# Kernel optimization log

Measured on AMD Instinct MI355X. Metric: run time of the kernel, lower is better.

The kernel has to match this reference:

```python
import jax, jax.numpy as jnp
import numpy as np

# Hyperparameters (from init_kwargs)
D_MODEL = 1024
D_STATE = 64
HEADDIM = 64
MIMO_RANK = 2
CHUNK = 128
EXPAND = 2
D_INNER = EXPAND * D_MODEL            # 2048
NHEADS = D_INNER // HEADDIM           # 32
G = MIMO_RANK * D_STATE               # effective state channels per head = 128
D_CONV = 4
D_XBC = D_INNER + 2 * NHEADS * G      # conv channels
D_IN_PROJ = 2 * D_INNER + 2 * NHEADS * G + NHEADS  # [z, x, B, C, dt]


def rmsnorm(x, w, eps=1e-5):
    return x * w * jax.lax.rsqrt(jnp.mean(x * x, axis=-1, keepdims=True) + eps)


def setup_inputs() -> dict:
    key = jax.random.key(0)
    ks = jax.random.split(key, 8)
    B, L = 2, 2048
    x = jax.random.normal(ks[0], (B, L, D_MODEL), jnp.float32)
    norm_w = jnp.ones((D_MODEL,), jnp.float32)
    in_proj_w = jax.random.normal(ks[1], (D_IN_PROJ, D_MODEL), jnp.float32) * 0.02
    conv_w = jax.random.normal(ks[2], (D_XBC, D_CONV), jnp.float32) * 0.2
    conv_b = jnp.zeros((D_XBC,), jnp.float32)
    dt_bias = jax.random.uniform(ks[3], (NHEADS,), jnp.float32, minval=-4.0, maxval=-1.0)
    A_log = jnp.log(jax.random.uniform(ks[4], (NHEADS,), jnp.float32, minval=1.0, maxval=8.0))
    D_skip = jnp.ones((NHEADS,), jnp.float32)
    gnorm_w = jnp.ones((D_INNER,), jnp.float32)
    out_proj_w = jax.random.normal(ks[5], (D_MODEL, D_INNER), jnp.float32) * 0.02
    return dict(x=x, norm_w=norm_w, in_proj_w=in_proj_w, conv_w=conv_w, conv_b=conv_b,
                dt_bias=dt_bias, A_log=A_log, D_skip=D_skip, gnorm_w=gnorm_w,
                out_proj_w=out_proj_w)


def _mamba3(u, in_proj_w, conv_w, conv_b, dt_bias, A_log, D_skip, gnorm_w, out_proj_w):
    B, L, _ = u.shape
    H, P = NHEADS, HEADDIM
    nc = L // CHUNK

    zxbcdt = u @ in_proj_w.T                                   # (B,L,D_IN_PROJ)
    z, xbc, dt_raw = jnp.split(zxbcdt, [D_INNER, D_INNER + D_XBC], axis=-1)

    # causal depthwise conv (width D_CONV) + SiLU on [x, B, C]
    xp = jnp.pad(xbc, ((0, 0), (D_CONV - 1, 0), (0, 0)))
    conv = conv_b + sum(xp[:, k:k + L, :] * conv_w[:, k] for k in range(D_CONV))
    xbc = jax.nn.silu(conv)
    xh, Bm, Cm = jnp.split(xbc, [D_INNER, D_INNER + H * G], axis=-1)

    Xc = xh.reshape(B, nc, CHUNK, H, P)
    Bc = Bm.reshape(B, nc, CHUNK, H, G)
    Cc = Cm.reshape(B, nc, CHUNK, H, G)

    dt = jax.nn.softplus(dt_raw + dt_bias)                     # (B,L,H), positive
    A = -jnp.exp(A_log)                                        # (H,), negative
    dtc = dt.reshape(B, nc, CHUNK, H)
    a = dtc * A                                                # log decay, (B,nc,cs,H)
    cum = jnp.cumsum(a, axis=2)                                # inclusive cumsum within chunk

    # intra-chunk (quadratic, causal) part
    cumT = cum.transpose(0, 1, 3, 2)                           # (B,nc,H,cs)
    diff = cumT[..., :, None] - cumT[..., None, :]             # cum_l - cum_s
    mask = jnp.tril(jnp.ones((CHUNK, CHUNK), bool))
    decay = jnp.where(mask, jnp.exp(jnp.where(mask, diff, 0.0)), 0.0)
    dtT = dtc.transpose(0, 1, 3, 2)                            # (B,nc,H,cs)
    scores = jnp.einsum('bclhg,bcshg->bchls', Cc, Bc) * decay * dtT[:, :, :, None, :]
    Y_intra = jnp.einsum('bchls,bcshp->bclhp', scores, Xc)

    # inter-chunk state recurrence
    w = jnp.exp(cum[:, :, -1:, :] - cum) * dtc                 # (B,nc,cs,H)
    S = jnp.einsum('bcshg,bcshp->bchgp', Bc * w[..., None], Xc)  # chunk states
    dlast = jnp.exp(cum[:, :, -1, :])                          # (B,nc,H) total chunk decay

    def step(carry, inp):
        dl, s = inp
        return dl[:, :, None, None] * carry + s, carry

    init = jnp.zeros((B, H, G, P), u.dtype)
    _, Hprev = jax.lax.scan(step, init, (dlast.transpose(1, 0, 2), S.transpose(1, 0, 2, 3, 4)))
    Hprev = Hprev.transpose(1, 0, 2, 3, 4)                     # (B,nc,H,G,P) state before chunk
    Y_inter = jnp.einsum('bclhg,bchgp->bclhp', Cc * jnp.exp(cum)[..., None], Hprev)

    y = (Y_intra + Y_inter + D_skip[:, None] * Xc).reshape(B, L, D_INNER)
    y = rmsnorm(y * jax.nn.silu(z), gnorm_w)                   # gated RMSNorm
    return y @ out_proj_w.T


def reference(x, norm_w, in_proj_w, conv_w, conv_b, dt_bias, A_log, D_skip, gnorm_w, out_proj_w):
    # pre-norm residual wrapper
    return x + _mamba3(rmsnorm(x, norm_w), in_proj_w, conv_w, conv_b,
                       dt_bias, A_log, D_skip, gnorm_w, out_proj_w)
```

## Files before the change

kernel.cpp:

```cpp
#include <hip/hip_runtime.h>

typedef unsigned short u16;
typedef __attribute__((ext_vector_type(8))) short bf16x8;
typedef __attribute__((ext_vector_type(4))) float f32x4;

#define MFMA16(a,b,c) __builtin_amdgcn_mfma_f32_16x16x32_bf16(a,b,c,0,0,0)

#define DMODEL   1024
#define DINNER   2048
#define NHEADS   32
#define HEADDIM  64
#define GDIM     128
#define DXBC     10240
#define DPROJ    12320
#define CHUNK_L  128
#define NCHUNK   16
#define NROWS    4096

__device__ __forceinline__ float b2f(u16 u){ return __uint_as_float(((unsigned)u)<<16); }
__device__ __forceinline__ u16 f2b(float f){
  unsigned u = __float_as_uint(f);
  u += 0x7fffu + ((u>>16)&1u);
  return (u16)(u>>16);
}

__device__ __forceinline__ void gload_lds16(const void* g, void* l){
  __builtin_amdgcn_global_load_lds(
      (const __attribute__((address_space(1))) unsigned int*)g,
      (__attribute__((address_space(3))) unsigned int*)l, 16, 0, 0);
}

__global__ __launch_bounds__(256) void k_prep(const float* __restrict__ s1, u16* __restrict__ d1, int n1,
                                              const float* __restrict__ s2, u16* __restrict__ d2, int n2,
                                              const float* __restrict__ x, const float* __restrict__ w,
                                              u16* __restrict__ u){
  __shared__ float red[4];
  if (blockIdx.x < 2048){
    int i = blockIdx.x*256 + threadIdx.x;
    int stride = 2048*256;
    int t1 = n1 >> 2, t2 = n2 >> 2;
    for (int j=i; j<t1+t2; j+=stride){
      const float4* sp; uint2* dp; int idx;
      if (j < t1){ sp = (const float4*)s1; dp = (uint2*)d1; idx = j; }
      else       { sp = (const float4*)s2; dp = (uint2*)d2; idx = j - t1; }
      float4 v = sp[idx];
      uint2 o;
      o.x = (unsigned)f2b(v.x) | ((unsigned)f2b(v.y)<<16);
      o.y = (unsigned)f2b(v.z) | ((unsigned)f2b(v.w)<<16);
      dp[idx] = o;
    }
  } else {
    int row = blockIdx.x - 2048, tid = threadIdx.x;
    float4 v = reinterpret_cast<const float4*>(x + (size_t)row*DMODEL)[tid];
    float ss = v.x*v.x + v.y*v.y + v.z*v.z + v.w*v.w;
    #pragma unroll
    for (int off=32; off>0; off>>=1) ss += __shfl_down(ss, off, 64);
    if ((tid&63)==0) red[tid>>6] = ss;
    __syncthreads();
    float tot = red[0]+red[1]+red[2]+red[3];
    float sc = rsqrtf(tot/(float)DMODEL + 1e-5f);
    float4 wv = reinterpret_cast<const float4*>(w)[tid];
    uint2 o;
    o.x = (unsigned)f2b(v.x*wv.x*sc) | ((unsigned)f2b(v.y*wv.y*sc)<<16);
    o.y = (unsigned)f2b(v.z*wv.z*sc) | ((unsigned)f2b(v.w*wv.w*sc)<<16);
    reinterpret_cast<uint2*>(u + (size_t)row*DMODEL)[tid] = o;
  }
}

__global__ __launch_bounds__(512) void k_gemm1_8p(const u16* __restrict__ A,
                                                  const u16* __restrict__ W,
                                                  u16* __restrict__ zb,
                                                  u16* __restrict__ xbc){
  __shared__ __align__(16) u16 lds[65536];
  const int tid  = threadIdx.x;
  const int lane = tid & 63, w = tid >> 6;
  const int wr = w >> 2, wc = w & 3;
  int bid = blockIdx.x;
  int xcd = bid & 7, g = bid >> 3;
  int st  = xcd*6 + (g >> 4);
  int wi  = g & 15;
  int tm  = (st/12)*4 + (wi>>2);
  int tn  = (st%12)*4 + (wi&3);
  const int m0 = tm*256, n0 = tn*256;

  const int srow = w*8 + (lane>>3);
  const int scol = ((lane&7) ^ ((lane>>3)&7))*8;
  const u16* aS = A + (size_t)(m0 + srow)*DMODEL + scol;
  const u16* bS = W + (size_t)(n0 + srow)*DMODEL + scol;
  const int ldsw = w*512;

  const int rr = lane & 15, gq = lane >> 4;

  f32x4 acc[8][4];
  #pragma unroll
  for (int i=0;i<8;i++)
    #pragma unroll
    for (int j=0;j<4;j++) acc[i][j] = (f32x4){0,0,0,0};

  auto SU_A = [&](int kt, int j){
    gload_lds16(aS + (size_t)(j*64)*DMODEL + kt*64,
                lds + (kt&1)*32768 + j*4096 + ldsw);
  };
  auto SU_B = [&](int kt, int j){
    gload_lds16(bS + (size_t)(j*64)*DMODEL + kt*64,
                lds + (kt&1)*32768 + 16384 + j*4096 + ldsw);
  };

  SU_A(0,0); SU_A(0,2); SU_B(0,0); SU_B(0,2); SU_B(0,1); SU_B(0,3); SU_A(0,1); SU_A(0,3);
  asm volatile("s_waitcnt vmcnt(2)" ::: "memory");
  __builtin_amdgcn_s_barrier();
  __builtin_amdgcn_sched_barrier(0);

  for (int kt = 0; kt < 16; ++kt){
    const u16* bufA = lds + (kt&1)*32768;
    const u16* bufB = bufA + 16384;
    const bool stg = (kt < 15);
    bf16x8 af[4][2], bw0[2][2], bw1[2][2];

    auto RDA = [&](int ti, int ks)->bf16x8{
      int r = wr*128 + ti*16 + rr;
      int s = (ks*4 + gq) ^ (rr & 7);
      return *(const bf16x8*)&bufA[r*64 + s*8];
    };
    auto RDB = [&](int tj, int ks)->bf16x8{
      int r = wc*64 + tj*16 + rr;
      int s = (ks*4 + gq) ^ (rr & 7);
      return *(const bf16x8*)&bufB[r*64 + s*8];
    };

    #pragma unroll
    for (int ti=0;ti<4;ti++){ af[ti][0]=RDA(ti,0); af[ti][1]=RDA(ti,1); }
    #pragma unroll
    for (int tj=0;tj<2;tj++){ bw0[tj][0]=RDB(tj,0); bw0[tj][1]=RDB(tj,1); }
    if (stg){ SU_A(kt+1,0); SU_A(kt+1,2); }
    __builtin_amdgcn_s_barrier();
    asm volatile("s_waitcnt lgkmcnt(0)" ::: "memory");
    __builtin_amdgcn_sched_barrier(0);
    __builtin_amdgcn_s_setprio(1);
    #pragma unroll
    for (int ti=0;ti<4;ti++)
      #pragma unroll
      for (int tj=0;tj<2;tj++){
        acc[ti][tj] = MFMA16(af[ti][0], bw0[tj][0], acc[ti][tj]);
        acc[ti][tj] = MFMA16(af[ti][1], bw0[tj][1], acc[ti][tj]);
      }
    __builtin_amdgcn_s_setprio(0);
    __builtin_amdgcn_s_barrier();

    #pragma unroll
    for (int tj=0;tj<2;tj++){ bw1[tj][0]=RDB(tj+2,0); bw1[tj][1]=RDB(tj+2,1); }
    if (stg){ SU_B(kt+1,0); SU_B(kt+1,2); }
    __builtin_amdgcn_s_barrier();
    asm volatile("s_waitcnt lgkmcnt(0)" ::: "memory");
    __builtin_amdgcn_sched_barrier(0);
    __builtin_amdgcn_s_setprio(1);
    #pragma unroll
    for (int ti=0;ti<4;ti++)
      #pragma unroll
      for (int tj=0;tj<2;tj++){
        acc[ti][tj+2] = MFMA16(af[ti][0], bw1[tj][0], acc[ti][tj+2]);
        acc[ti][tj+2] = MFMA16(af[ti][1], bw1[tj][1], acc[ti][tj+2]);
      }
    __builtin_amdgcn_s_setprio(0);
    if (stg) asm volatile("s_waitcnt vmcnt(4)" ::: "memory");
    else     asm volatile("s_waitcnt vmcnt(0)" ::: "memory");
    __builtin_amdgcn_s_barrier();

    #pragma unroll
    for (int ti=0;ti<4;ti++){ af[ti][0]=RDA(ti+4,0); af[ti][1]=RDA(ti+4,1); }
    if (stg){ SU_B(kt+1,1); SU_B(kt+1,3); }
    __builtin_amdgcn_s_barrier();
    asm volatile("s_waitcnt lgkmcnt(0)" ::: "memory");
    __builtin_amdgcn_sched_barrier(0);
    __builtin_amdgcn_s_setprio(1);
    #pragma unroll
    for (int ti=0;ti<4;ti++)
      #pragma unroll
      for (int tj=0;tj<2;tj++){
        acc[4+ti][tj] = MFMA16(af[ti][0], bw0[tj][0], acc[4+ti][tj]);
        acc[4+ti][tj] = MFMA16(af[ti][1], bw0[tj][1], acc[4+ti][tj]);
      }
    __builtin_amdgcn_s_setprio(0);
    __builtin_amdgcn_s_barrier();

    if (stg){ SU_A(kt+1,1); SU_A(kt+1,3); }
    __builtin_amdgcn_s_barrier();
    __builtin_amdgcn_sched_barrier(0);
    __builtin_amdgcn_s_setprio(1);
    #pragma unroll
    for (int ti=0;ti<4;ti++)
      #pragma unroll
      for (int tj=0;tj<2;tj++){
        acc[4+ti][tj+2] = MFMA16(af[ti][0], bw1[tj][0], acc[4+ti][tj+2]);
        acc[4+ti][tj+2] = MFMA16(af[ti][1], bw1[tj][1], acc[4+ti][tj+2]);
      }
    __builtin_amdgcn_s_setprio(0);
    if (stg){
      asm volatile("s_waitcnt vmcnt(2)" ::: "memory");
      __builtin_amdgcn_s_barrier();
      __builtin_amdgcn_sched_barrier(0);
    }
  }

  const int row0 = m0 + wr*128 + (lane>>4)*4;
  const int colb = wc*64 + (lane&15);
  if (tn >= 8){
    const int cb = n0 - DINNER;
    #pragma unroll
    for (int ti=0;ti<8;ti++)
      #pragma unroll
      for (int tj=0;tj<4;tj++)
        #pragma unroll
        for (int q=0;q<4;q++)
          xbc[(size_t)(row0 + ti*16 + q)*DXBC + cb + colb + tj*16] = f2b(acc[ti][tj][q]);
  } else {
    #pragma unroll
    for (int ti=0;ti<8;ti++)
      #pragma unroll
      for (int tj=0;tj<4;tj++)
        #pragma unroll
        for (int q=0;q<4;q++)
          zb[(size_t)(row0 + ti*16 + q)*DINNER + n0 + colb + tj*16] = f2b(acc[ti][tj][q]);
  }
}

__global__ __launch_bounds__(256) void k_gemm_dt(const u16* __restrict__ A,
                                                 const u16* __restrict__ W,
                                                 float* __restrict__ dtraw){
  const int lane = threadIdx.x & 63, wv = threadIdx.x >> 6;
  const int m0 = blockIdx.x*32;
  const int n0 = DINNER + DXBC;
  const int r  = lane & 15;
  const int kb = (lane>>4)*8;
  const int k0 = wv*256;
  const u16* a0p = A + (size_t)(m0 + r)*DMODEL + k0 + kb;
  const u16* a1p = a0p + 16*DMODEL;
  const u16* b0p = W + (size_t)(n0 + r)*DMODEL + k0 + kb;
  const u16* b1p = b0p + 16*DMODEL;
  f32x4 acc00={0,0,0,0}, acc01={0,0,0,0}, acc10={0,0,0,0}, acc11={0,0,0,0};
  #pragma unroll
  for (int k=0;k<256;k+=32){
    bf16x8 a0 = *(const bf16x8*)(a0p + k);
    bf16x8 a1 = *(const bf16x8*)(a1p + k);
    bf16x8 b0 = *(const bf16x8*)(b0p + k);
    bf16x8 b1 = *(const bf16x8*)(b1p + k);
    acc00 = MFMA16(a0,b0,acc00);
    acc01 = MFMA16(a0,b1,acc01);
    acc10 = MFMA16(a1,b0,acc10);
    acc11 = MFMA16(a1,b1,acc11);
  }
  __shared__ float part[4][1024];
  int rowb = (lane>>4)*4, col = lane&15;
  #pragma unroll
  for (int rr=0; rr<4; rr++){
    part[wv][(rowb+rr)*32 + col]         = acc00[rr];
    part[wv][(rowb+rr)*32 + col+16]      = acc01[rr];
    part[wv][(rowb+16+rr)*32 + col]      = acc10[rr];
    part[wv][(rowb+16+rr)*32 + col+16]   = acc11[rr];
  }
  __syncthreads();
  int idx = threadIdx.x*4;
  #pragma unroll
  for (int q=0;q<4;q++){
    int i = idx+q;
    dtraw[(size_t)m0*NHEADS + i] = part[0][i]+part[1][i]+part[2][i]+part[3][i];
  }
}

__global__ __launch_bounds__(256) void k_convdt(const u16* __restrict__ xbc,
                                                const float* __restrict__ cw,
                                                const float* __restrict__ cb,
                                                u16* __restrict__ xh,
                                                u16* __restrict__ Bm,
                                                u16* __restrict__ Cm,
                                                const float* __restrict__ dtraw,
                                                const float* __restrict__ dt_bias,
                                                const float* __restrict__ A_log,
                                                float* __restrict__ dtT,
                                                float* __restrict__ cumT){
  __shared__ float lds2[2][128];
  int tid = threadIdx.x;
  if (blockIdx.x < 2560){
    int cblk = blockIdx.x;
    int cx = cblk % 10, ry = cblk / 10;
    int c0 = (cx*256 + tid)*4;
    int row0 = ry*16;
    int l0 = row0 & 2047;
    float4 w4[4]; float cbv[4];
    #pragma unroll
    for (int j=0;j<4;j++){ w4[j] = reinterpret_cast<const float4*>(cw)[c0+j]; cbv[j] = cb[c0+j]; }
    float p3[4]={0,0,0,0}, p2[4]={0,0,0,0}, p1[4]={0,0,0,0};
    auto loadquad = [&](int rw, float q[4]){
      uint2 v = *(const uint2*)&xbc[(size_t)rw*DXBC + c0];
      const u16* pv = (const u16*)&v;
      #pragma unroll
      for (int j=0;j<4;j++) q[j] = b2f(pv[j]);
    };
    if (l0 >= 3){ loadquad(row0-3,p3); loadquad(row0-2,p2); loadquad(row0-1,p1); }
    #pragma unroll
    for (int i=0;i<16;i++){
      float cur[4]; loadquad(row0+i, cur);
      float o[4];
      #pragma unroll
      for (int j=0;j<4;j++){
        float s = cbv[j] + p3[j]*w4[j].x + p2[j]*w4[j].y + p1[j]*w4[j].z + cur[j]*w4[j].w;
        o[j] = s/(1.f+expf(-s));
      }
      uint2 ov;
      ov.x = (unsigned)f2b(o[0]) | ((unsigned)f2b(o[1])<<16);
      ov.y = (unsigned)f2b(o[2]) | ((unsigned)f2b(o[3])<<16);
      int rw = row0 + i;
      if (c0 < DINNER)            *(uint2*)&xh[(size_t)rw*DINNER + c0] = ov;
      else if (c0 < DINNER+4096)  *(uint2*)&Bm[(size_t)rw*4096 + (c0-DINNER)] = ov;
      else                        *(uint2*)&Cm[(size_t)rw*4096 + (c0-DINNER-4096)] = ov;
      #pragma unroll
      for (int j=0;j<4;j++){ p3[j]=p2[j]; p2[j]=p1[j]; p1[j]=cur[j]; }
    }
  } else {
    int half = tid >> 7;
    int blk  = (blockIdx.x - 2560)*2 + half;
    int h  = blk & 31;
    int bc = blk >> 5;
    int s  = tid & 127;
    int row = bc*128 + s;
    float xv = dtraw[(size_t)row*NHEADS + h] + dt_bias[h];
    float dt = (xv > 20.f) ? xv : log1pf(expf(xv));
    float a  = dt * (-expf(A_log[h]));
    lds2[half][s] = a; __syncthreads();
    #pragma unroll
    for (int off=1; off<128; off<<=1){
      float t = (s>=off) ? lds2[half][s-off] : 0.f;
      __syncthreads();
      lds2[half][s] += t;
      __syncthreads();
    }
    dtT[(size_t)blk*128 + s]  = dt;
    cumT[(size_t)blk*128 + s] = lds2[half][s];
  }
}

__global__ __launch_bounds__(512) void k_states(const u16* __restrict__ Bm,
                                                const u16* __restrict__ xh,
                                                const float* __restrict__ dtT,
                                                const float* __restrict__ cumT,
                                                u16* __restrict__ S){
  int blk = blockIdx.x;
  int h = blk & 31, bc = blk >> 5;
  __shared__ __align__(16) u16 Bw[128][136];
  __shared__ __align__(16) u16 XT[64][136];
  __shared__ float cum[128], dtv[128];
  int tid = threadIdx.x;
  if (tid < 128){ cum[tid] = cumT[(size_t)blk*128+tid]; dtv[tid] = dtT[(size_t)blk*128+tid]; }
  __syncthreads();
  float clast = cum[127];
  #pragma unroll
  for (int it=0; it<4; ++it){
    int s  = it*32 + (tid>>4);
    int g8 = (tid&15)*8;
    uint4 v = *(const uint4*)&Bm[(size_t)(bc*128+s)*4096 + h*128 + g8];
    float w = expf(clast - cum[s]) * dtv[s];
    const u16* pv = (const u16*)&v;
    #pragma unroll
    for (int j=0;j<8;j++) Bw[g8+j][s] = f2b(b2f(pv[j]) * w);
  }
  #pragma unroll
  for (int it=0; it<4; ++it){
    int s  = it*32 + (tid>>4);
    int p4 = (tid&15)*4;
    uint2 v = *(const uint2*)&xh[(size_t)(bc*128+s)*DINNER + h*64 + p4];
    const u16* pv = (const u16*)&v;
    #pragma unroll
    for (int j=0;j<4;j++) XT[p4+j][s] = pv[j];
  }
  __syncthreads();
  int lane = tid & 63, wv = tid >> 6;
  int r = lane & 15, kb = (lane>>4)*8;
  f32x4 acc[4];
  #pragma unroll
  for (int j=0;j<4;j++) acc[j] = (f32x4){0,0,0,0};
  #pragma unroll
  for (int k=0;k<128;k+=32){
    bf16x8 a0 = *(const bf16x8*)&Bw[wv*16 + r][k+kb];
    #pragma unroll
    for (int tj=0;tj<4;tj++){
      bf16x8 bb = *(const bf16x8*)&XT[tj*16 + r][k+kb];
      acc[tj] = MFMA16(a0,bb,acc[tj]);
    }
  }
  u16* Sp = S + (size_t)blk*8192;
  int g0 = wv*16 + (lane>>4)*4, p0 = lane&15;
  #pragma unroll
  for (int tj=0;tj<4;tj++)
    #pragma unroll
    for (int rr=0;rr<4;rr++)
      Sp[(g0 + rr)*64 + tj*16 + p0] = f2b(acc[tj][rr]);
}

__global__ __launch_bounds__(256) void k_scan(const u16* __restrict__ S,
                                              const float* __restrict__ cumT,
                                              u16* __restrict__ Hp){
  int slice = blockIdx.x & 3;
  int bh = blockIdx.x >> 2;
  int b = bh >> 5, h = bh & 31;
  int e0 = slice*2048 + threadIdx.x*8;
  float c8[8];
  #pragma unroll
  for (int j=0;j<8;j++) c8[j] = 0.f;
  int blk0 = (b*16+0)*32 + h;
  uint4 sv = *(const uint4*)&S[(size_t)blk0*8192 + e0];
  float dl = expf(cumT[(size_t)blk0*128 + 127]);
  for (int c=0;c<NCHUNK;c++){
    int blkn = (b*16+c+1)*32 + h;
    uint4 nx; float dln = 0.f;
    if (c < NCHUNK-1){
      nx  = *(const uint4*)&S[(size_t)blkn*8192 + e0];
      dln = expf(cumT[(size_t)blkn*128 + 127]);
    }
    int blk = (b*16+c)*32 + h;
    const u16* sp = (const u16*)&sv;
    uint4 o; u16* op = (u16*)&o;
    #pragma unroll
    for (int j=0;j<8;j++) op[j] = f2b(c8[j]);
    *reinterpret_cast<uint4*>(&Hp[(size_t)blk*8192 + e0]) = o;
    #pragma unroll
    for (int j=0;j<8;j++) c8[j] = dl*c8[j] + b2f(sp[j]);
    sv = nx; dl = dln;
  }
}

__global__ __launch_bounds__(512) void k_intra(const u16* __restrict__ Cm,
                                               const u16* __restrict__ Bm,
                                               const u16* __restrict__ xh,
                                               const u16* __restrict__ Hp,
                                               const float* __restrict__ dtT,
                                               const float* __restrict__ cumT,
                                               const float* __restrict__ Dskip,
                                               u16* __restrict__ yh){
  int blk = blockIdx.x;
  int h = blk & 31, bc = blk >> 5;
  __shared__ __align__(16) u16 Bl[128][136];
  __shared__ __align__(16) u16 XT[64][136];
  __shared__ __align__(16) u16 HT[64][136];
  __shared__ float cum[128], dtv[128];
  int tid = threadIdx.x;
  int lane = tid & 63, wv = tid >> 6;
  int r = lane & 15, kb = (lane>>4)*8;

  bf16x8 cfr[4];
  {
    const u16* cp = Cm + (size_t)(bc*128 + wv*16 + r)*4096 + h*128 + kb;
    #pragma unroll
    for (int ks=0;ks<4;ks++) cfr[ks] = *(const bf16x8*)(cp + ks*32);
  }

  if (tid < 128){ cum[tid] = cumT[(size_t)blk*128+tid]; dtv[tid] = dtT[(size_t)blk*128+tid]; }
  #pragma unroll
  for (int it=0; it<4; ++it){
    int rw = it*32 + (tid>>4);
    int g8 = (tid&15)*8;
    *(uint4*)&Bl[rw][g8] = *(const uint4*)&Bm[(size_t)(bc*128+rw)*4096 + h*128 + g8];
  }
  __syncthreads();

  uint2 xt[4], ht[4];
  #pragma unroll
  for (int it=0; it<4; ++it){
    int s  = it*32 + (tid>>4);
    int p4 = (tid&15)*4;
    xt[it] = *(const uint2*)&xh[(size_t)(bc*128+s)*DINNER + h*64 + p4];
    ht[it] = *(const uint2*)&Hp[(size_t)blk*8192 + (it*32 + (tid>>4))*64 + p4];
  }

  const int tjmax = wv;
  f32x4 p1[8];
  #pragma unroll
  for (int j=0;j<8;j++) p1[j] = (f32x4){0,0,0,0};
  #pragma unroll
  for (int ks=0;ks<4;ks++){
    bf16x8 a0 = cfr[ks];
    #pragma unroll
    for (int tj=0;tj<8;tj++){
      if (tj > tjmax) continue;
      bf16x8 bb = *(const bf16x8*)&Bl[tj*16 + r][ks*32+kb];
      p1[tj] = MFMA16(a0,bb,p1[tj]);
    }
  }
  #pragma unroll
  for (int it=0; it<4; ++it){
    int s  = it*32 + (tid>>4);
    int p4 = (tid&15)*4;
    const u16* pv = (const u16*)&xt[it];
    #pragma unroll
    for (int j=0;j<4;j++) XT[p4+j][s] = pv[j];
    const u16* ph = (const u16*)&ht[it];
    #pragma unroll
    for (int j=0;j<4;j++) HT[p4+j][it*32 + (tid>>4)] = ph[j];
  }
  __syncthreads();

  int row0 = wv*16 + (lane>>4)*4;
  #pragma unroll
  for (int tj=0;tj<8;tj++)
    #pragma unroll
    for (int rr=0;rr<4;rr++){
      int l = row0 + rr;
      int s = tj*16 + (lane&15);
      float v = p1[tj][rr];
      v = (s <= l) ? v * expf(cum[l]-cum[s]) * dtv[s] : 0.f;
      Bl[l][s] = f2b(v);
    }
  __syncthreads();

  f32x4 y[4];
  #pragma unroll
  for (int j=0;j<4;j++) y[j] = (f32x4){0,0,0,0};
  #pragma unroll
  for (int ks=0;ks<4;ks++){
    bf16x8 a0 = cfr[ks];
    #pragma unroll
    for (int tj=0;tj<4;tj++){
      bf16x8 bb = *(const bf16x8*)&HT[tj*16 + r][ks*32+kb];
      y[tj] = MFMA16(a0,bb,y[tj]);
    }
  }
  #pragma unroll
  for (int rr=0;rr<4;rr++){
    float e = expf(cum[row0 + rr]);
    #pragma unroll
    for (int tj=0;tj<4;tj++) y[tj][rr] *= e;
  }
  #pragma unroll
  for (int k=0;k<128;k+=32){
    bf16x8 a0 = *(const bf16x8*)&Bl[wv*16 + r][k+kb];
    #pragma unroll
    for (int tj=0;tj<4;tj++){
      bf16x8 bb = *(const bf16x8*)&XT[tj*16 + r][k+kb];
      y[tj] = MFMA16(a0,bb,y[tj]);
    }
  }
  float Dh = Dskip[h];
  #pragma unroll
  for (int tj=0;tj<4;tj++)
    #pragma unroll
    for (int rr=0;rr<4;rr++){
      int l = row0 + rr;
      int p = tj*16 + (lane&15);
      float xv = b2f(XT[p][l]);
      yh[(size_t)(bc*128 + l)*DINNER + h*64 + p] = f2b(y[tj][rr] + Dh*xv);
    }
}

__global__ __launch_bounds__(256) void k_gate(const u16* __restrict__ yh,
                                              const u16* __restrict__ zb,
                                              const float* __restrict__ gw,
                                              u16* __restrict__ out){
  int row = blockIdx.x, tid = threadIdx.x;
  const uint4 yv = reinterpret_cast<const uint4*>(yh + (size_t)row*DINNER)[tid];
  const uint4 zv = reinterpret_cast<const uint4*>(zb + (size_t)row*DINNER)[tid];
  const unsigned* yp = (const unsigned*)&yv;
  const unsigned* zp = (const unsigned*)&zv;
  float t[8]; float ss = 0.f;
  #pragma unroll
  for (int i=0;i<4;i++){
    float y0 = b2f((u16)yp[i]), y1 = b2f((u16)(yp[i]>>16));
    float z0 = b2f((u16)zp[i]), z1 = b2f((u16)(zp[i]>>16));
    float v0 = y0 * (z0 / (1.f + expf(-z0)));
    float v1 = y1 * (z1 / (1.f + expf(-z1)));
    t[2*i] = v0; t[2*i+1] = v1; ss += v0*v0 + v1*v1;
  }
  #pragma unroll
  for (int off=32; off>0; off>>=1) ss += __shfl_down(ss, off, 64);
  __shared__ float red[4];
  if ((tid&63)==0) red[tid>>6] = ss;
  __syncthreads();
  float tot = red[0]+red[1]+red[2]+red[3];
  float g = rsqrtf(tot/(float)DINNER + 1e-5f);
  const float4 g0 = reinterpret_cast<const float4*>(gw)[tid*2];
  const float4 g1 = reinterpret_cast<const float4*>(gw)[tid*2+1];
  uint4 o;
  unsigned* op = (unsigned*)&o;
  float gg[8] = {g0.x,g0.y,g0.z,g0.w,g1.x,g1.y,g1.z,g1.w};
  #pragma unroll
  for (int i=0;i<4;i++)
    op[i] = (unsigned)f2b(t[2*i]*gg[2*i]*g) | ((unsigned)f2b(t[2*i+1]*gg[2*i+1]*g)<<16);
  reinterpret_cast<uint4*>(out + (size_t)row*DINNER)[tid] = o;
}

__global__ __launch_bounds__(256) void k_gemm2_64(const u16* __restrict__ A,
                                                  const u16* __restrict__ W,
                                                  const float* __restrict__ xres,
                                                  float* __restrict__ out){
  __shared__ __align__(16) u16 lds[2*16384];
  const int tid  = threadIdx.x;
  const int lane = tid & 63, wv = tid >> 6;
  const int wr = wv >> 1, wc = wv & 1;
  const int NWG = 8*32, Q = NWG/8;
  int swz = (blockIdx.x & 7)*Q + (blockIdx.x >> 3);
  int tm = swz / 8, tn = swz % 8;
  int m0 = tm*128, n0 = tn*128;
  const int K = DINNER;

  const int srow = tid >> 3;
  const int sslot = ((tid&7) ^ ((tid>>3)&7))*8;
  const u16* aSrc = A + (size_t)(m0 + srow)*K + sslot;
  const u16* bSrc = W + (size_t)(n0 + srow)*K + sslot;
  const int ldsu = wv*512;

  const int rr = lane & 15, gq = lane >> 4;

  f32x4 acc[4][4];
  #pragma unroll
  for (int i=0;i<4;i++)
    #pragma unroll
    for (int j=0;j<4;j++) acc[i][j] = (f32x4){0,0,0,0};

  auto STAGE = [&](int kt){
    u16* base = lds + (kt&1)*16384;
    #pragma unroll
    for (int j=0;j<4;j++)
      gload_lds16(aSrc + (size_t)(j*32)*K + kt*64, base + j*2048 + ldsu);
    #pragma unroll
    for (int j=0;j<4;j++)
      gload_lds16(bSrc + (size_t)(j*32)*K + kt*64, base + 8192 + j*2048 + ldsu);
  };
  auto KSTEP = [&](int kt, bool stg){
    const u16* bufA = lds + (kt&1)*16384;
    const u16* bufB = bufA + 8192;
    bf16x8 af[4][2], bw[4][2];
    #pragma unroll
    for (int t=0;t<4;t++){
      #pragma unroll
      for (int ks=0;ks<2;ks++){
        int sa = (ks*4 + gq) ^ (rr & 7);
        af[t][ks] = *(const bf16x8*)&bufA[(wr*64 + t*16 + rr)*64 + sa*8];
        bw[t][ks] = *(const bf16x8*)&bufB[(wc*64 + t*16 + rr)*64 + sa*8];
      }
    }
    asm volatile("s_waitcnt lgkmcnt(0)" ::: "memory");
    __builtin_amdgcn_s_barrier();
    if (stg) STAGE(kt+2);
    __builtin_amdgcn_s_setprio(1);
    #pragma unroll
    for (int ti=0;ti<4;ti++)
      #pragma unroll
      for (int tj=0;tj<4;tj++){
        acc[ti][tj] = MFMA16(af[ti][0], bw[tj][0], acc[ti][tj]);
        acc[ti][tj] = MFMA16(af[ti][1], bw[tj][1], acc[ti][tj]);
      }
    __builtin_amdgcn_s_setprio(0);
  };

  STAGE(0); STAGE(1);
  asm volatile("s_waitcnt vmcnt(8)" ::: "memory");
  __builtin_amdgcn_s_barrier();
  __builtin_amdgcn_sched_barrier(0);
  const int NT = K/64;
  for (int kt = 0; kt < NT-2; ++kt){
    KSTEP(kt, true);
    asm volatile("s_waitcnt vmcnt(8)" ::: "memory");
    __builtin_amdgcn_s_barrier();
    __builtin_amdgcn_sched_barrier(0);
  }
  KSTEP(NT-2, false);
  asm volatile("s_waitcnt vmcnt(0)" ::: "memory");
  __builtin_amdgcn_s_barrier();
  __builtin_amdgcn_sched_barrier(0);
  KSTEP(NT-1, false);

  int row0 = m0 + wr*64 + (lane>>4)*4;
  int col0 = n0 + wc*64 + (lane&15);
  #pragma unroll
  for (int ti=0;ti<4;ti++)
    #pragma unroll
    for (int tj=0;tj<4;tj++)
      #pragma unroll
      for (int q=0;q<4;q++){
        size_t idx = (size_t)(row0+ti*16+q)*DMODEL + col0 + tj*16;
        out[idx] = acc[ti][tj][q] + xres[idx];
      }
}

extern "C" void kernel_launch(void* const* d_in, const int* in_sizes, int n_in,
                              void* d_out, int out_size, void* d_ws, size_t ws_size,
                              hipStream_t stream) {
  (void)in_sizes; (void)n_in; (void)out_size; (void)ws_size;
  const float* x         = (const float*)d_in[0];
  const float* norm_w    = (const float*)d_in[1];
  const float* in_proj_w = (const float*)d_in[2];
  const float* conv_w    = (const float*)d_in[3];
  const float* conv_b    = (const float*)d_in[4];
  const float* dt_bias   = (const float*)d_in[5];
  const float* A_log     = (const float*)d_in[6];
  const float* D_skip    = (const float*)d_in[7];
  const float* gnorm_w   = (const float*)d_in[8];
  const float* out_proj_w= (const float*)d_in[9];
  float* out = (float*)d_out;

  char* ws = (char*)d_ws;
  size_t off = 0;
  auto alloc = [&](size_t bytes)->char*{
    char* p = ws + off; off = (off + bytes + 255) & ~(size_t)255; return p;
  };
  u16*   W2    = (u16*)  alloc((size_t)DMODEL*DINNER*2);
  u16*   zb    = (u16*)  alloc((size_t)NROWS*DINNER*2);
  float* dtraw = (float*)alloc((size_t)NROWS*NHEADS*4);
  float* dtT   = (float*)alloc((size_t)1024*128*4);
  float* cumT  = (float*)alloc((size_t)1024*128*4);
  u16*   xhb   = (u16*)  alloc((size_t)NROWS*DINNER*2);
  u16*   Bmb   = (u16*)  alloc((size_t)NROWS*4096*2);
  u16*   Cmb   = (u16*)  alloc((size_t)NROWS*4096*2);
  char*  R1    = alloc((size_t)NROWS*DXBC*2);
  u16*   xbcr  = (u16*)R1;
  u16*   S     = (u16*)R1;
  u16*   Hp    = (u16*)(R1 + (size_t)1024*8192*4);
  u16*   yh    = (u16*)R1;
  char*  R2    = alloc((size_t)DPROJ*DMODEL*2 + (size_t)NROWS*DMODEL*2);
  u16*   W1    = (u16*)R2;
  u16*   u_bf  = (u16*)(R2 + (size_t)DPROJ*DMODEL*2);
  u16*   gated = (u16*)R2;

  k_prep<<<2048+NROWS,256,0,stream>>>(in_proj_w, W1, DPROJ*DMODEL,
                                      out_proj_w, W2, DMODEL*DINNER,
                                      x, norm_w, u_bf);
  k_gemm_dt<<<NROWS/32,256,0,stream>>>(u_bf, W1, dtraw);
  k_gemm1_8p<<<768,512,0,stream>>>(u_bf, W1, zb, xbcr);
  k_convdt<<<2560+512,256,0,stream>>>(xbcr, conv_w, conv_b, xhb, Bmb, Cmb,
                                      dtraw, dt_bias, A_log, dtT, cumT);
  k_states<<<1024,512,0,stream>>>(Bmb, xhb, dtT, cumT, S);
  k_scan<<<256,256,0,stream>>>(S, cumT, Hp);
  k_intra<<<1024,512,0,stream>>>(Cmb, Bmb, xhb, Hp, dtT, cumT, D_skip, yh);
  k_gate<<<NROWS,256,0,stream>>>(yh, zb, gnorm_w, gated);
  k_gemm2_64<<<8*32,256,0,stream>>>(gated, W2, x, out);
}
```

Baseline: 288.0 us.

## Fuse causal conv and SiLU into in_proj GEMM epilogue via LDS tile

The in_proj GEMM epilogue now stages each 256x256 xBC output tile in swizzled LDS and applies the depthwise causal conv plus SiLU directly, writing xh/B/C. This avoids writing and re-reading the full raw xBC activation through global memory. Rows whose conv window crosses a tile boundary (the first three of each tile) are fixed up in a small separate kernel, using boundary rows saved to a side buffer. The fused epilogue does its serial per-column conv loop with strided, uncoalesced global stores and an extra barrier, which may lengthen the GEMM tail.

Result: slower. 417.2 us (+44.8%).

```diff
diff --git a/kernel.cpp b/kernel.cpp
--- a/kernel.cpp
+++ b/kernel.cpp
@@ -70,7 +70,12 @@
 __global__ __launch_bounds__(512) void k_gemm1_8p(const u16* __restrict__ A,
                                                   const u16* __restrict__ W,
                                                   u16* __restrict__ zb,
-                                                  u16* __restrict__ xbc){
+                                                  u16* __restrict__ xh,
+                                                  u16* __restrict__ Bm,
+                                                  u16* __restrict__ Cm,
+                                                  const float* __restrict__ cw,
+                                                  const float* __restrict__ cb,
+                                                  u16* __restrict__ sideRaw){
   __shared__ __align__(16) u16 lds[65536];
   const int tid  = threadIdx.x;
   const int lane = tid & 63, w = tid >> 6;
@@ -202,18 +207,9 @@
     }
   }
 
-  const int row0 = m0 + wr*128 + (lane>>4)*4;
-  const int colb = wc*64 + (lane&15);
-  if (tn >= 8){
-    const int cb = n0 - DINNER;
-    #pragma unroll
-    for (int ti=0;ti<8;ti++)
-      #pragma unroll
-      for (int tj=0;tj<4;tj++)
-        #pragma unroll
-        for (int q=0;q<4;q++)
-          xbc[(size_t)(row0 + ti*16 + q)*DXBC + cb + colb + tj*16] = f2b(acc[ti][tj][q]);
-  } else {
+  if (tn < 8){
+    const int row0 = m0 + wr*128 + (lane>>4)*4;
+    const int colb = wc*64 + (lane&15);
     #pragma unroll
     for (int ti=0;ti<8;ti++)
       #pragma unroll
@@ -221,6 +217,54 @@
         #pragma unroll
         for (int q=0;q<4;q++)
           zb[(size_t)(row0 + ti*16 + q)*DINNER + n0 + colb + tj*16] = f2b(acc[ti][tj][q]);
+    return;
+  }
+
+  const int cb0 = n0 - DINNER;
+  #pragma unroll
+  for (int ti=0;ti<8;ti++)
+    #pragma unroll
+    for (int tj=0;tj<4;tj++)
+      #pragma unroll
+      for (int q=0;q<4;q++){
+        int rl = wr*128 + ti*16 + (lane>>4)*4 + q;
+        int cl = wc*64 + tj*16 + (lane&15);
+        lds[rl*256 + (cl ^ (((rl>>2)&3)<<4))] = f2b(acc[ti][tj][q]);
+      }
+  __syncthreads();
+
+  #pragma unroll
+  for (int it=0; it<3; ++it){
+    int idx = tid + it*512;
+    int r6  = idx >> 8;
+    int c   = idx & 255;
+    int rl  = (r6 < 3) ? r6 : (250 + r6);
+    sideRaw[((size_t)tm*6 + r6)*DXBC + cb0 + c] = lds[rl*256 + (c ^ (((rl>>2)&3)<<4))];
+  }
+
+  {
+    int c    = tid & 255;
+    int half = tid >> 8;
+    int gc   = cb0 + c;
+    float4 w4 = reinterpret_cast<const float4*>(cw)[gc];
+    float cbv = cb[gc];
+    u16* outp; int ostride;
+    if (gc < DINNER){ outp = xh + gc; ostride = DINNER; }
+    else if (gc < DINNER+4096){ outp = Bm + (gc - DINNER); ostride = 4096; }
+    else { outp = Cm + (gc - DINNER - 4096); ostride = 4096; }
+    auto TRD = [&](int l)->float {
+      return b2f(lds[l*256 + (c ^ (((l>>2)&3)<<4))]);
+    };
+    int lstart = half ? 128 : 3;
+    int lend   = half ? 256 : 128;
+    float p3 = TRD(lstart-3), p2 = TRD(lstart-2), p1 = TRD(lstart-1);
+    for (int l=lstart; l<lend; ++l){
+      float cur = TRD(l);
+      float s = cbv + p3*w4.x + p2*w4.y + p1*w4.z + cur*w4.w;
+      s = s/(1.f+expf(-s));
+      outp[(size_t)(m0+l)*ostride] = f2b(s);
+      p3=p2; p2=p1; p1=cur;
+    }
   }
 }
 
@@ -267,58 +311,48 @@
   }
 }
 
-__global__ __launch_bounds__(256) void k_convdt(const u16* __restrict__ xbc,
-                                                const float* __restrict__ cw,
-                                                const float* __restrict__ cb,
-                                                u16* __restrict__ xh,
-                                                u16* __restrict__ Bm,
-                                                u16* __restrict__ Cm,
-                                                const float* __restrict__ dtraw,
-                                                const float* __restrict__ dt_bias,
-                                                const float* __restrict__ A_log,
-                                                float* __restrict__ dtT,
-                                                float* __restrict__ cumT){
+__global__ __launch_bounds__(256) void k_fixdt(const u16* __restrict__ sideRaw,
+                                               const float* __restrict__ cw,
+                                               const float* __restrict__ cb,
+                                               u16* __restrict__ xh,
+                                               u16* __restrict__ Bm,
+                                               u16* __restrict__ Cm,
+                                               const float* __restrict__ dtraw,
+                                               const float* __restrict__ dt_bias,
+                                               const float* __restrict__ A_log,
+                                               float* __restrict__ dtT,
+                                               float* __restrict__ cumT){
   __shared__ float lds2[2][128];
   int tid = threadIdx.x;
-  if (blockIdx.x < 2560){
-    int cblk = blockIdx.x;
-    int cx = cblk % 10, ry = cblk / 10;
-    int c0 = (cx*256 + tid)*4;
-    int row0 = ry*16;
-    int l0 = row0 & 2047;
-    float4 w4[4]; float cbv[4];
-    #pragma unroll
-    for (int j=0;j<4;j++){ w4[j] = reinterpret_cast<const float4*>(cw)[c0+j]; cbv[j] = cb[c0+j]; }
-    float p3[4]={0,0,0,0}, p2[4]={0,0,0,0}, p1[4]={0,0,0,0};
-    auto loadquad = [&](int rw, float q[4]){
-      uint2 v = *(const uint2*)&xbc[(size_t)rw*DXBC + c0];
-      const u16* pv = (const u16*)&v;
-      #pragma unroll
-      for (int j=0;j<4;j++) q[j] = b2f(pv[j]);
-    };
-    if (l0 >= 3){ loadquad(row0-3,p3); loadquad(row0-2,p2); loadquad(row0-1,p1); }
-    #pragma unroll
-    for (int i=0;i<16;i++){
-      float cur[4]; loadquad(row0+i, cur);
-      float o[4];
-      #pragma unroll
-      for (int j=0;j<4;j++){
-        float s = cbv[j] + p3[j]*w4[j].x + p2[j]*w4[j].y + p1[j]*w4[j].z + cur[j]*w4[j].w;
-        o[j] = s/(1.f+expf(-s));
-      }
-      uint2 ov;
-      ov.x = (unsigned)f2b(o[0]) | ((unsigned)f2b(o[1])<<16);
-      ov.y = (unsigned)f2b(o[2]) | ((unsigned)f2b(o[3])<<16);
-      int rw = row0 + i;
-      if (c0 < DINNER)            *(uint2*)&xh[(size_t)rw*DINNER + c0] = ov;
-      else if (c0 < DINNER+4096)  *(uint2*)&Bm[(size_t)rw*4096 + (c0-DINNER)] = ov;
-      else                        *(uint2*)&Cm[(size_t)rw*4096 + (c0-DINNER-4096)] = ov;
-      #pragma unroll
-      for (int j=0;j<4;j++){ p3[j]=p2[j]; p2[j]=p1[j]; p1[j]=cur[j]; }
+  if (blockIdx.x < 16){
+    int tm = blockIdx.x;
+    int m0 = tm*256;
+    bool bstart = (m0 & 2047) == 0;
+    for (int it=0; it<120; ++it){
+      int idx = it*256 + tid;
+      int j  = idx / DXBC;
+      int gc = idx - j*DXBC;
+      float4 w4 = reinterpret_cast<const float4*>(cw)[gc];
+      const float* wk = (const float*)&w4;
+      float s = cb[gc];
+      #pragma unroll
+      for (int k=0;k<4;k++){
+        int i = j - 3 + k;
+        if (bstart && i < 0) continue;
+        u16 rv = (i >= 0) ? sideRaw[((size_t)tm*6 + i)*DXBC + gc]
+                          : sideRaw[((size_t)(tm-1)*6 + (i+6))*DXBC + gc];
+        s += b2f(rv) * wk[k];
+      }
+      s = s/(1.f+expf(-s));
+      u16 ov = f2b(s);
+      int rw = m0 + j;
+      if (gc < DINNER)            xh[(size_t)rw*DINNER + gc] = ov;
+      else if (gc < DINNER+4096)  Bm[(size_t)rw*4096 + (gc-DINNER)] = ov;
+      else                        Cm[(size_t)rw*4096 + (gc-DINNER-4096)] = ov;
     }
   } else {
     int half = tid >> 7;
-    int blk  = (blockIdx.x - 2560)*2 + half;
+    int blk  = (blockIdx.x - 16)*2 + half;
     int h  = blk & 31;
     int bc = blk >> 5;
     int s  = tid & 127;
@@ -709,8 +743,8 @@
   u16*   xhb   = (u16*)  alloc((size_t)NROWS*DINNER*2);
   u16*   Bmb   = (u16*)  alloc((size_t)NROWS*4096*2);
   u16*   Cmb   = (u16*)  alloc((size_t)NROWS*4096*2);
+  u16*   sideRaw=(u16*)  alloc((size_t)16*6*DXBC*2);
   char*  R1    = alloc((size_t)NROWS*DXBC*2);
-  u16*   xbcr  = (u16*)R1;
   u16*   S     = (u16*)R1;
   u16*   Hp    = (u16*)(R1 + (size_t)1024*8192*4);
   u16*   yh    = (u16*)R1;
@@ -723,9 +757,10 @@
                                       out_proj_w, W2, DMODEL*DINNER,
                                       x, norm_w, u_bf);
   k_gemm_dt<<<NROWS/32,256,0,stream>>>(u_bf, W1, dtraw);
-  k_gemm1_8p<<<768,512,0,stream>>>(u_bf, W1, zb, xbcr);
-  k_convdt<<<2560+512,256,0,stream>>>(xbcr, conv_w, conv_b, xhb, Bmb, Cmb,
-                                      dtraw, dt_bias, A_log, dtT, cumT);
+  k_gemm1_8p<<<768,512,0,stream>>>(u_bf, W1, zb, xhb, Bmb, Cmb,
+                                   conv_w, conv_b, sideRaw);
+  k_fixdt<<<16+512,256,0,stream>>>(sideRaw, conv_w, conv_b, xhb, Bmb, Cmb,
+                                   dtraw, dt_bias, A_log, dtT, cumT);
   k_states<<<1024,512,0,stream>>>(Bmb, xhb, dtT, cumT, S);
   k_scan<<<256,256,0,stream>>>(S, cumT, Hp);
   k_intra<<<1024,512,0,stream>>>(Cmb, Bmb, xhb, Hp, dtT, cumT, D_skip, yh);
```

## Stage GEMM epilogues through swizzled LDS and widen conv loads/stores

Applied to the files above, without the earlier changes.

The in-projection GEMM epilogue now writes its bf16 accumulators into LDS with an XOR swizzle, then each thread writes a full row segment with 16-byte vector stores instead of scattered 2-byte stores. The out-projection epilogue does the same in fp32, fusing the residual add with float4 loads and stores. The conv kernel processes 8 channels per thread with 16-byte accesses, halving its block count. This targets uncoalesced narrow global writes, at the cost of an extra LDS round trip, a barrier, and more registers per conv thread.

New measurement: 316.3 us. +9.8%, slower.

```diff
diff --git a/kernel.cpp b/kernel.cpp
--- a/kernel.cpp
+++ b/kernel.cpp
@@ -202,25 +202,30 @@
     }
   }
 
-  const int row0 = m0 + wr*128 + (lane>>4)*4;
-  const int colb = wc*64 + (lane&15);
-  if (tn >= 8){
-    const int cb = n0 - DINNER;
-    #pragma unroll
-    for (int ti=0;ti<8;ti++)
-      #pragma unroll
-      for (int tj=0;tj<4;tj++)
-        #pragma unroll
-        for (int q=0;q<4;q++)
-          xbc[(size_t)(row0 + ti*16 + q)*DXBC + cb + colb + tj*16] = f2b(acc[ti][tj][q]);
-  } else {
-    #pragma unroll
-    for (int ti=0;ti<8;ti++)
-      #pragma unroll
-      for (int tj=0;tj<4;tj++)
-        #pragma unroll
-        for (int q=0;q<4;q++)
-          zb[(size_t)(row0 + ti*16 + q)*DINNER + n0 + colb + tj*16] = f2b(acc[ti][tj][q]);
+  #pragma unroll
+  for (int ti=0;ti<8;ti++)
+    #pragma unroll
+    for (int tj=0;tj<4;tj++)
+      #pragma unroll
+      for (int q=0;q<4;q++){
+        int rl = wr*128 + ti*16 + (lane>>4)*4 + q;
+        int cl = wc*64 + tj*16 + (lane&15);
+        lds[rl*256 + (cl ^ ((rl&7)<<3))] = f2b(acc[ti][tj][q]);
+      }
+  __syncthreads();
+  u16* dst; size_t dstride; int dcol;
+  if (tn >= 8){ dst = xbc; dstride = DXBC;   dcol = n0 - DINNER; }
+  else        { dst = zb;  dstride = DINNER; dcol = n0; }
+  {
+    int r  = tid & 255;
+    int hb = (tid >> 8) * 128;
+    u16* drow = dst + (size_t)(m0 + r)*dstride + dcol + hb;
+    #pragma unroll
+    for (int i=0;i<16;i++){
+      int c = hb + i*8;
+      uint4 v = *(const uint4*)&lds[r*256 + (c ^ ((r&7)<<3))];
+      *(uint4*)&drow[i*8] = v;
+    }
   }
 }
 
@@ -280,45 +285,43 @@
                                                 float* __restrict__ cumT){
   __shared__ float lds2[2][128];
   int tid = threadIdx.x;
-  if (blockIdx.x < 2560){
+  if (blockIdx.x < 1280){
     int cblk = blockIdx.x;
-    int cx = cblk % 10, ry = cblk / 10;
-    int c0 = (cx*256 + tid)*4;
+    int cx = cblk % 5, ry = cblk / 5;
+    int c0 = (cx*256 + tid)*8;
     int row0 = ry*16;
     int l0 = row0 & 2047;
-    float4 w4[4]; float cbv[4];
-    #pragma unroll
-    for (int j=0;j<4;j++){ w4[j] = reinterpret_cast<const float4*>(cw)[c0+j]; cbv[j] = cb[c0+j]; }
-    float p3[4]={0,0,0,0}, p2[4]={0,0,0,0}, p1[4]={0,0,0,0};
-    auto loadquad = [&](int rw, float q[4]){
-      uint2 v = *(const uint2*)&xbc[(size_t)rw*DXBC + c0];
+    float4 w4[8]; float cbv[8];
+    #pragma unroll
+    for (int j=0;j<8;j++){ w4[j] = reinterpret_cast<const float4*>(cw)[c0+j]; cbv[j] = cb[c0+j]; }
+    float p3[8]={0,0,0,0,0,0,0,0}, p2[8]={0,0,0,0,0,0,0,0}, p1[8]={0,0,0,0,0,0,0,0};
+    auto loadoct = [&](int rw, float q[8]){
+      uint4 v = *(const uint4*)&xbc[(size_t)rw*DXBC + c0];
       const u16* pv = (const u16*)&v;
       #pragma unroll
-      for (int j=0;j<4;j++) q[j] = b2f(pv[j]);
+      for (int j=0;j<8;j++) q[j] = b2f(pv[j]);
     };
-    if (l0 >= 3){ loadquad(row0-3,p3); loadquad(row0-2,p2); loadquad(row0-1,p1); }
+    if (l0 >= 3){ loadoct(row0-3,p3); loadoct(row0-2,p2); loadoct(row0-1,p1); }
     #pragma unroll
     for (int i=0;i<16;i++){
-      float cur[4]; loadquad(row0+i, cur);
-      float o[4];
-      #pragma unroll
-      for (int j=0;j<4;j++){
+      float cur[8]; loadoct(row0+i, cur);
+      u16 o[8];
+      #pragma unroll
+      for (int j=0;j<8;j++){
         float s = cbv[j] + p3[j]*w4[j].x + p2[j]*w4[j].y + p1[j]*w4[j].z + cur[j]*w4[j].w;
-        o[j] = s/(1.f+expf(-s));
-      }
-      uint2 ov;
-      ov.x = (unsigned)f2b(o[0]) | ((unsigned)f2b(o[1])<<16);
-      ov.y = (unsigned)f2b(o[2]) | ((unsigned)f2b(o[3])<<16);
+        o[j] = f2b(s/(1.f+expf(-s)));
+      }
+      uint4 ov = *(const uint4*)o;
       int rw = row0 + i;
-      if (c0 < DINNER)            *(uint2*)&xh[(size_t)rw*DINNER + c0] = ov;
-      else if (c0 < DINNER+4096)  *(uint2*)&Bm[(size_t)rw*4096 + (c0-DINNER)] = ov;
-      else                        *(uint2*)&Cm[(size_t)rw*4096 + (c0-DINNER-4096)] = ov;
-      #pragma unroll
-      for (int j=0;j<4;j++){ p3[j]=p2[j]; p2[j]=p1[j]; p1[j]=cur[j]; }
+      if (c0 < DINNER)            *(uint4*)&xh[(size_t)rw*DINNER + c0] = ov;
+      else if (c0 < DINNER+4096)  *(uint4*)&Bm[(size_t)rw*4096 + (c0-DINNER)] = ov;
+      else                        *(uint4*)&Cm[(size_t)rw*4096 + (c0-DINNER-4096)] = ov;
+      #pragma unroll
+      for (int j=0;j<8;j++){ p3[j]=p2[j]; p2[j]=p1[j]; p1[j]=cur[j]; }
     }
   } else {
     int half = tid >> 7;
-    int blk  = (blockIdx.x - 2560)*2 + half;
+    int blk  = (blockIdx.x - 1280)*2 + half;
     int h  = blk & 31;
     int bc = blk >> 5;
     int s  = tid & 127;
@@ -667,17 +670,32 @@
   __builtin_amdgcn_sched_barrier(0);
   KSTEP(NT-1, false);
 
-  int row0 = m0 + wr*64 + (lane>>4)*4;
-  int col0 = n0 + wc*64 + (lane&15);
+  float* fl = (float*)lds;
   #pragma unroll
   for (int ti=0;ti<4;ti++)
     #pragma unroll
     for (int tj=0;tj<4;tj++)
       #pragma unroll
       for (int q=0;q<4;q++){
-        size_t idx = (size_t)(row0+ti*16+q)*DMODEL + col0 + tj*16;
-        out[idx] = acc[ti][tj][q] + xres[idx];
-      }
+        int rl = wr*64 + ti*16 + (lane>>4)*4 + q;
+        int cl = wc*64 + tj*16 + (lane&15);
+        fl[rl*128 + (cl ^ ((rl&7)<<2))] = acc[ti][tj][q];
+      }
+  __syncthreads();
+  {
+    int r  = tid & 127;
+    int hb = (tid >> 7) * 64;
+    const float* xr = xres + (size_t)(m0 + r)*DMODEL + n0 + hb;
+    float* orow = out + (size_t)(m0 + r)*DMODEL + n0 + hb;
+    #pragma unroll
+    for (int i=0;i<16;i++){
+      int c = hb + i*4;
+      float4 v = *(const float4*)&fl[r*128 + (c ^ ((r&7)<<2))];
+      float4 xv = *(const float4*)&xr[i*4];
+      v.x += xv.x; v.y += xv.y; v.z += xv.z; v.w += xv.w;
+      *(float4*)&orow[i*4] = v;
+    }
+  }
 }
 
 extern "C" void kernel_launch(void* const* d_in, const int* in_sizes, int n_in,
@@ -724,7 +742,7 @@
                                       x, norm_w, u_bf);
   k_gemm_dt<<<NROWS/32,256,0,stream>>>(u_bf, W1, dtraw);
   k_gemm1_8p<<<768,512,0,stream>>>(u_bf, W1, zb, xbcr);
-  k_convdt<<<2560+512,256,0,stream>>>(xbcr, conv_w, conv_b, xhb, Bmb, Cmb,
+  k_convdt<<<1280+512,256,0,stream>>>(xbcr, conv_w, conv_b, xhb, Bmb, Cmb,
                                       dtraw, dt_bias, A_log, dtT, cumT);
   k_states<<<1024,512,0,stream>>>(Bmb, xhb, dtT, cumT, S);
   k_scan<<<256,256,0,stream>>>(S, cumT, Hp);
```
